# Optimization experiments

Measured on AMD Instinct MI355X. Metric: run time of the kernel, lower is better.

Reference implementation:

```python
import jax, jax.numpy as jnp
import numpy as np

N = 524288            # total ray samples
EMB_DIM = 32          # hash embedder out_dim (16 levels x 2 feats)
DIR_DIM = 27          # freq embedder out_dim (3 + 3*2*4)
GEO_FEAT = 15         # cfg.geo_feature_dim
LATENT_DIM = 128      # cfg.latent_code_dim
NUM_LATENT = 100      # cfg.num_latent_code
D_HIDDEN = 64
RGB_IN = EMB_DIM + DIR_DIM + GEO_FEAT + LATENT_DIM  # 202


def setup_inputs() -> dict:
    key = jax.random.key(0)
    ks = jax.random.split(key, 16)

    def lin(k, fan_in, fan_out):
        # torch nn.Linear default init: U(-1/sqrt(fan_in), 1/sqrt(fan_in))
        bound = 1.0 / np.sqrt(fan_in)
        kw, kb = jax.random.split(k)
        W = jax.random.uniform(kw, (fan_in, fan_out), jnp.float32, -bound, bound)
        b = jax.random.uniform(kb, (fan_out,), jnp.float32, -bound, bound)
        return W, b

    occ_W0, occ_b0 = lin(ks[0], EMB_DIM, D_HIDDEN)
    occ_W1, occ_b1 = lin(ks[1], D_HIDDEN, D_HIDDEN)
    occ_W2, occ_b2 = lin(ks[2], D_HIDDEN, 1 + GEO_FEAT)
    rgb_W0, rgb_b0 = lin(ks[3], RGB_IN, D_HIDDEN)
    rgb_W1, rgb_b1 = lin(ks[4], D_HIDDEN, D_HIDDEN)
    rgb_W2, rgb_b2 = lin(ks[5], D_HIDDEN, 3)

    # kaiming_normal_ init of rgb_latent
    rgb_latent = jax.random.normal(ks[6], (NUM_LATENT, LATENT_DIM), jnp.float32) * np.sqrt(2.0 / LATENT_DIM)

    embedded = jax.random.normal(ks[7], (N, EMB_DIM), jnp.float32)
    embedded_dir = jax.random.normal(ks[8], (N, DIR_DIM), jnp.float32)

    return {
        'embedded': embedded, 'embedded_dir': embedded_dir,
        'occ_W0': occ_W0, 'occ_b0': occ_b0,
        'occ_W1': occ_W1, 'occ_b1': occ_b1,
        'occ_W2': occ_W2, 'occ_b2': occ_b2,
        'rgb_W0': rgb_W0, 'rgb_b0': rgb_b0,
        'rgb_W1': rgb_W1, 'rgb_b1': rgb_b1,
        'rgb_W2': rgb_W2, 'rgb_b2': rgb_b2,
        'rgb_latent': rgb_latent,
        'latent_index': 7,
    }


def reference(embedded, embedded_dir,
              occ_W0, occ_b0, occ_W1, occ_b1, occ_W2, occ_b2,
              rgb_W0, rgb_b0, rgb_W1, rgb_b1, rgb_W2, rgb_b2,
              rgb_latent, latent_index):
    sp = jax.nn.softplus
    # occ MLP: softplus hidden layers, linear output
    h = sp(embedded @ occ_W0 + occ_b0)
    h = sp(h @ occ_W1 + occ_b1)
    hidden = h @ occ_W2 + occ_b2                     # [N, 1+GEO_FEAT]
    occ = 1.0 - jnp.exp(-sp(hidden[:, :1]))          # [N, 1]
    feature = hidden[:, 1:]                          # [N, GEO_FEAT]
    # latent gather: one latent code broadcast over all N samples
    n = embedded.shape[0]
    latent = jnp.broadcast_to(rgb_latent[latent_index], (n, rgb_latent.shape[1]))
    x = jnp.concatenate([embedded, embedded_dir, feature, latent], axis=-1)  # [N, 202]
    # rgb MLP
    r = sp(x @ rgb_W0 + rgb_b0)
    r = sp(r @ rgb_W1 + rgb_b1)
    rgb = jax.nn.sigmoid(r @ rgb_W2 + rgb_b2)        # [N, 3]
    raw = jnp.concatenate([rgb, occ], axis=-1)       # [N, 4]
    return raw, occ
```

## Files before the change

### kernel.cpp

```cpp
#include <hip/hip_runtime.h>

typedef __bf16 bf16x8 __attribute__((ext_vector_type(8)));
typedef float f32x4 __attribute__((ext_vector_type(4)));
typedef unsigned int u32x4 __attribute__((ext_vector_type(4)));
typedef unsigned int u32x2 __attribute__((ext_vector_type(2)));
typedef u32x4 u32x4a __attribute__((may_alias));
typedef u32x2 u32x2a __attribute__((may_alias));
typedef f32x4 f32x4a __attribute__((may_alias));

#define NITER 8

__device__ inline unsigned short f2b(float f) {
    unsigned int x;
    __builtin_memcpy(&x, &f, 4);
    unsigned int r = (x + 0x7FFFu + ((x >> 16) & 1u)) >> 16;
    return (unsigned short)r;
}
__device__ inline unsigned int cvt_pk_bf16(float lo, float hi) {
    unsigned int r;
    asm("v_cvt_pk_bf16_f32 %0, %1, %2" : "=v"(r) : "v"(lo), "v"(hi));
    return r;
}
__device__ inline float softplus_f(float x) {
    return fmaxf(x, 0.f) + __logf(1.f + __expf(-fabsf(x)));
}
__device__ inline bf16x8 as_bf16x8(u32x4 v) { return __builtin_bit_cast(bf16x8, v); }


__global__ __launch_bounds__(256) void prep_weights(
    const float* __restrict__ oW0, const float* __restrict__ ob0,
    const float* __restrict__ oW1, const float* __restrict__ ob1,
    const float* __restrict__ oW2, const float* __restrict__ ob2,
    const float* __restrict__ rW0, const float* __restrict__ rb0,
    const float* __restrict__ rW1, const float* __restrict__ rb1,
    const float* __restrict__ rW2, const float* __restrict__ rb2,
    const float* __restrict__ rlat, const int* __restrict__ lidx,
    float* __restrict__ wsf, ushort* __restrict__ wsw)
{
    const int tid = threadIdx.x;
    for (int i = tid; i < 224; i += 256) {
        float v;
        if (i < 64)       v = ob0[i];
        else if (i < 128) v = ob1[i - 64];
        else if (i < 144) v = ob2[i - 128];
        else if (i < 208) v = rb1[i - 144];
        else              v = (i - 208 < 3) ? rb2[i - 208] : 0.f;
        wsf[i] = v;
    }
    if (tid < 64) {
        float acc = rb0[tid];
        const float* lat = rlat + (size_t)lidx[0] * 128;
        for (int k = 0; k < 128; k++)
            acc = fmaf(lat[k], rW0[(74 + k) * 64 + tid], acc);
        wsf[224 + tid] = acc;
    }
    for (int s = tid; s < 36 * 64; s += 256) {
        const int frag = s >> 6, lane = s & 63;
        const int qq = lane >> 4, cc = lane & 15;
        const float* W;
        int ldn = 64, nt = 0, kt = 0;
        bool isr0 = false, isr2 = false;
        if (frag < 4)       { W = oW0; nt = frag; kt = 0; }
        else if (frag < 12) { W = oW1; int f = frag - 4;  nt = f >> 1; kt = f & 1; }
        else if (frag < 14) { W = oW2; ldn = 16; nt = 0; kt = frag - 12; }
        else if (frag < 26) { W = rW0; int f = frag - 14; nt = f / 3; kt = f - nt * 3; isr0 = true; }
        else if (frag < 34) { W = rW1; int f = frag - 26; nt = f >> 1; kt = f & 1; }
        else                { W = rW2; ldn = 3; nt = 0; kt = frag - 34; isr2 = true; }
        const int nn = nt * 16 + cc;
        __align__(16) ushort vals[8];
#pragma unroll
        for (int j = 0; j < 8; j++) {
            int k = kt * 32 + qq * 8 + j;
            float v = 0.f;
            if (isr0) {
                int ks = -1;
                if (k < 59) ks = k;
                else if (k >= 64 && k < 79) ks = k - 5;
                if (ks >= 0) v = W[ks * 64 + nn];
            } else if (isr2) {
                if (nn < 3) v = W[k * 3 + nn];
            } else {
                v = W[k * ldn + nn];
            }
            vals[j] = f2b(v);
        }
        *(u32x4a*)&wsw[s * 8] = *(const u32x4a*)vals;
    }
}

__global__ __launch_bounds__(512, 4) void net_mfma(
    const float* __restrict__ emb, const float* __restrict__ dir,
    const float* __restrict__ wsf, const ushort* __restrict__ wsw,
    float* __restrict__ out, int n)
{
    __shared__ __align__(16) ushort s_w[36 * 64 * 8];
    __shared__ __align__(16) float  s_bias[288];
    __shared__ __align__(16) ushort s_h[8][16 * 72];
    __shared__ __align__(16) ushort s_feat[8][16 * 24];

    const int tid = threadIdx.x;
    for (int i = tid; i < 36 * 64; i += 512)
        *(u32x4a*)&s_w[i * 8] = *(const u32x4a*)(wsw + i * 8);
    for (int i = tid; i < 288; i += 512)
        s_bias[i] = wsf[i];
    __syncthreads();

    const int wave = tid >> 6, lane = tid & 63, q = lane >> 4, c = lane & 15;
    ushort* hw = s_h[wave];
    ushort* fw = s_feat[wave];
    if (lane < 16) fw[lane * 24 + 15] = 0;

    for (int it = 0; it < NITER; ++it) {
        const long p0 = (long)blockIdx.x * 1024 + it * 128 + wave * 16;

        bf16x8 x_emb, x_dir;
        {
            const float* ep = emb + (p0 + c) * 32 + q * 8;
            f32x4 e0 = *(const f32x4a*)ep;
            f32x4 e1 = *(const f32x4a*)(ep + 4);
            u32x4 pk = {cvt_pk_bf16(e0[0], e0[1]), cvt_pk_bf16(e0[2], e0[3]),
                        cvt_pk_bf16(e1[0], e1[1]), cvt_pk_bf16(e1[2], e1[3])};
            x_emb = as_bf16x8(pk);
        }
        {
            const float* dp = dir + (p0 + c) * 27;
            float dv[8];
#pragma unroll
            for (int j = 0; j < 8; j++) {
                int kl = q * 8 + j;
                dv[j] = (kl < 27) ? dp[kl] : 0.f;
            }
            u32x4 pk = {cvt_pk_bf16(dv[0], dv[1]), cvt_pk_bf16(dv[2], dv[3]),
                        cvt_pk_bf16(dv[4], dv[5]), cvt_pk_bf16(dv[6], dv[7])};
            x_dir = as_bf16x8(pk);
        }

#pragma unroll
        for (int nt = 0; nt < 4; ++nt) {
            f32x4 acc = *(const f32x4a*)&s_bias[0 + nt * 16 + q * 4];
            acc = __builtin_amdgcn_mfma_f32_16x16x32_bf16(
                as_bf16x8(*(const u32x4a*)&s_w[((0 + nt) * 64 + lane) * 8]), x_emb, acc, 0, 0, 0);
            u32x2 pk = {cvt_pk_bf16(softplus_f(acc[0]), softplus_f(acc[1])),
                        cvt_pk_bf16(softplus_f(acc[2]), softplus_f(acc[3]))};
            *(u32x2a*)&hw[c * 72 + nt * 16 + q * 4] = pk;
        }
        {
            bf16x8 h0 = as_bf16x8(*(const u32x4a*)&hw[c * 72 + 0 + q * 8]);
            bf16x8 h1 = as_bf16x8(*(const u32x4a*)&hw[c * 72 + 32 + q * 8]);
#pragma unroll
            for (int nt = 0; nt < 4; ++nt) {
                f32x4 acc = *(const f32x4a*)&s_bias[64 + nt * 16 + q * 4];
                acc = __builtin_amdgcn_mfma_f32_16x16x32_bf16(
                    as_bf16x8(*(const u32x4a*)&s_w[((4 + nt * 2 + 0) * 64 + lane) * 8]), h0, acc, 0, 0, 0);
                acc = __builtin_amdgcn_mfma_f32_16x16x32_bf16(
                    as_bf16x8(*(const u32x4a*)&s_w[((4 + nt * 2 + 1) * 64 + lane) * 8]), h1, acc, 0, 0, 0);
                u32x2 pk = {cvt_pk_bf16(softplus_f(acc[0]), softplus_f(acc[1])),
                            cvt_pk_bf16(softplus_f(acc[2]), softplus_f(acc[3]))};
                *(u32x2a*)&hw[c * 72 + nt * 16 + q * 4] = pk;
            }
        }
        float occv;
        {
            bf16x8 h0 = as_bf16x8(*(const u32x4a*)&hw[c * 72 + 0 + q * 8]);
            bf16x8 h1 = as_bf16x8(*(const u32x4a*)&hw[c * 72 + 32 + q * 8]);
            f32x4 acc = *(const f32x4a*)&s_bias[128 + q * 4];
            acc = __builtin_amdgcn_mfma_f32_16x16x32_bf16(
                as_bf16x8(*(const u32x4a*)&s_w[(12 * 64 + lane) * 8]), h0, acc, 0, 0, 0);
            acc = __builtin_amdgcn_mfma_f32_16x16x32_bf16(
                as_bf16x8(*(const u32x4a*)&s_w[(13 * 64 + lane) * 8]), h1, acc, 0, 0, 0);
            occv = 1.f - __expf(-softplus_f(acc[0]));
#pragma unroll
            for (int r = 0; r < 4; r++) {
                int o = q * 4 + r;
                if (o > 0) fw[c * 24 + o - 1] = f2b(acc[r]);
            }
        }
        {
            u32x4 rawf = *(const u32x4a*)&fw[c * 24 + q * 8];
            if (q >= 2) rawf = u32x4{0, 0, 0, 0};
            bf16x8 x_feat = as_bf16x8(rawf);
#pragma unroll
            for (int nt = 0; nt < 4; ++nt) {
                f32x4 acc = *(const f32x4a*)&s_bias[224 + nt * 16 + q * 4];
                acc = __builtin_amdgcn_mfma_f32_16x16x32_bf16(
                    as_bf16x8(*(const u32x4a*)&s_w[((14 + nt * 3 + 0) * 64 + lane) * 8]), x_emb, acc, 0, 0, 0);
                acc = __builtin_amdgcn_mfma_f32_16x16x32_bf16(
                    as_bf16x8(*(const u32x4a*)&s_w[((14 + nt * 3 + 1) * 64 + lane) * 8]), x_dir, acc, 0, 0, 0);
                acc = __builtin_amdgcn_mfma_f32_16x16x32_bf16(
                    as_bf16x8(*(const u32x4a*)&s_w[((14 + nt * 3 + 2) * 64 + lane) * 8]), x_feat, acc, 0, 0, 0);
                u32x2 pk = {cvt_pk_bf16(softplus_f(acc[0]), softplus_f(acc[1])),
                            cvt_pk_bf16(softplus_f(acc[2]), softplus_f(acc[3]))};
                *(u32x2a*)&hw[c * 72 + nt * 16 + q * 4] = pk;
            }
        }
        {
            bf16x8 h0 = as_bf16x8(*(const u32x4a*)&hw[c * 72 + 0 + q * 8]);
            bf16x8 h1 = as_bf16x8(*(const u32x4a*)&hw[c * 72 + 32 + q * 8]);
#pragma unroll
            for (int nt = 0; nt < 4; ++nt) {
                f32x4 acc = *(const f32x4a*)&s_bias[144 + nt * 16 + q * 4];
                acc = __builtin_amdgcn_mfma_f32_16x16x32_bf16(
                    as_bf16x8(*(const u32x4a*)&s_w[((26 + nt * 2 + 0) * 64 + lane) * 8]), h0, acc, 0, 0, 0);
                acc = __builtin_amdgcn_mfma_f32_16x16x32_bf16(
                    as_bf16x8(*(const u32x4a*)&s_w[((26 + nt * 2 + 1) * 64 + lane) * 8]), h1, acc, 0, 0, 0);
                u32x2 pk = {cvt_pk_bf16(softplus_f(acc[0]), softplus_f(acc[1])),
                            cvt_pk_bf16(softplus_f(acc[2]), softplus_f(acc[3]))};
                *(u32x2a*)&hw[c * 72 + nt * 16 + q * 4] = pk;
            }
        }
        {
            bf16x8 h0 = as_bf16x8(*(const u32x4a*)&hw[c * 72 + 0 + q * 8]);
            bf16x8 h1 = as_bf16x8(*(const u32x4a*)&hw[c * 72 + 32 + q * 8]);
            f32x4 acc = *(const f32x4a*)&s_bias[208 + q * 4];
            acc = __builtin_amdgcn_mfma_f32_16x16x32_bf16(
                as_bf16x8(*(const u32x4a*)&s_w[(34 * 64 + lane) * 8]), h0, acc, 0, 0, 0);
            acc = __builtin_amdgcn_mfma_f32_16x16x32_bf16(
                as_bf16x8(*(const u32x4a*)&s_w[(35 * 64 + lane) * 8]), h1, acc, 0, 0, 0);
            if (q == 0) {
                f32x4 o;
                o[0] = 1.f / (1.f + __expf(-acc[0]));
                o[1] = 1.f / (1.f + __expf(-acc[1]));
                o[2] = 1.f / (1.f + __expf(-acc[2]));
                o[3] = occv;
                *(f32x4a*)&out[(p0 + c) * 4] = o;
                out[(long)4 * n + p0 + c] = occv;
            }
        }
    }
}

extern "C" void kernel_launch(void* const* d_in, const int* in_sizes, int n_in,
                              void* d_out, int out_size, void* d_ws, size_t ws_size,
                              hipStream_t stream) {
    const int n = in_sizes[0] / 32;
    float*  wsf = (float*)d_ws;
    ushort* wsw = (ushort*)((char*)d_ws + 1152);
    prep_weights<<<1, 256, 0, stream>>>(
        (const float*)d_in[2], (const float*)d_in[3],
        (const float*)d_in[4], (const float*)d_in[5],
        (const float*)d_in[6], (const float*)d_in[7],
        (const float*)d_in[8], (const float*)d_in[9],
        (const float*)d_in[10], (const float*)d_in[11],
        (const float*)d_in[12], (const float*)d_in[13],
        (const float*)d_in[14], (const int*)d_in[15],
        wsf, wsw);
    net_mfma<<<n / 1024, 512, 0, stream>>>(
        (const float*)d_in[0], (const float*)d_in[1],
        wsf, wsw, (float*)d_out, n);
}
```

Baseline: 235.5 us.

## Streamline activations, keep biases in registers, vectorize dir loads, parallelize weight prep

Replaces softplus and sigmoid with raw v_exp/v_log/v_rcp intrinsics and computes occupancy as sigmoid(x), using the identity 1-exp(-softplus(x)) = sigmoid(x). Biases move from LDS into registers. The feature vector is repacked in place in the hidden buffer by shifting the rgb_W0 layout, which removes the separate feature LDS buffer. The direction loads become vectorized float4 loads with a bounds fallback, and weight prep is spread over 8 blocks with a split reduction for the latent dot product. The unguarded softplus form log2(1+exp2(x)) can overflow for large inputs, and the extra bias registers raise register pressure.

```diff
diff --git a/kernel.cpp b/kernel.cpp
--- a/kernel.cpp
+++ b/kernel.cpp
@@ -7,6 +7,7 @@
 typedef u32x4 u32x4a __attribute__((may_alias));
 typedef u32x2 u32x2a __attribute__((may_alias));
 typedef f32x4 f32x4a __attribute__((may_alias));
+typedef unsigned int u32a __attribute__((may_alias));
 
 #define NITER 8
 
@@ -21,8 +22,14 @@
     asm("v_cvt_pk_bf16_f32 %0, %1, %2" : "=v"(r) : "v"(lo), "v"(hi));
     return r;
 }
+__device__ inline float vexp2(float x) { float r; asm("v_exp_f32 %0, %1" : "=v"(r) : "v"(x)); return r; }
+__device__ inline float vlog2(float x) { float r; asm("v_log_f32 %0, %1" : "=v"(r) : "v"(x)); return r; }
+__device__ inline float vrcp(float x)  { float r; asm("v_rcp_f32 %0, %1" : "=v"(r) : "v"(x)); return r; }
 __device__ inline float softplus_f(float x) {
-    return fmaxf(x, 0.f) + __logf(1.f + __expf(-fabsf(x)));
+    return 0.69314718f * vlog2(1.f + vexp2(1.44269504f * x));
+}
+__device__ inline float sigmoid_f(float x) {
+    return vrcp(1.f + vexp2(-1.44269504f * x));
 }
 __device__ inline bf16x8 as_bf16x8(u32x4 v) { return __builtin_bit_cast(bf16x8, v); }
 
@@ -37,24 +44,33 @@
     const float* __restrict__ rlat, const int* __restrict__ lidx,
     float* __restrict__ wsf, ushort* __restrict__ wsw)
 {
-    const int tid = threadIdx.x;
-    for (int i = tid; i < 224; i += 256) {
-        float v;
-        if (i < 64)       v = ob0[i];
-        else if (i < 128) v = ob1[i - 64];
-        else if (i < 144) v = ob2[i - 128];
-        else if (i < 208) v = rb1[i - 144];
-        else              v = (i - 208 < 3) ? rb2[i - 208] : 0.f;
-        wsf[i] = v;
-    }
-    if (tid < 64) {
-        float acc = rb0[tid];
+    const int bid = blockIdx.x, tid = threadIdx.x;
+    __shared__ float red[256];
+
+    if (bid == 0) {
+        for (int i = tid; i < 224; i += 256) {
+            float v;
+            if (i < 64)       v = ob0[i];
+            else if (i < 128) v = ob1[i - 64];
+            else if (i < 144) v = ob2[i - 128];
+            else if (i < 208) v = rb1[i - 144];
+            else              v = (i - 208 < 3) ? rb2[i - 208] : 0.f;
+            wsf[i] = v;
+        }
+    }
+    if (bid == 7) {
+        const int outn = tid & 63, sl = tid >> 6;
         const float* lat = rlat + (size_t)lidx[0] * 128;
-        for (int k = 0; k < 128; k++)
-            acc = fmaf(lat[k], rW0[(74 + k) * 64 + tid], acc);
-        wsf[224 + tid] = acc;
-    }
-    for (int s = tid; s < 36 * 64; s += 256) {
+        float p = 0.f;
+        for (int k = sl * 32; k < sl * 32 + 32; k++)
+            p = fmaf(lat[k], rW0[(74 + k) * 64 + outn], p);
+        red[tid] = p;
+        __syncthreads();
+        if (tid < 64)
+            wsf[224 + tid] = rb0[tid] + red[tid] + red[64 + tid] + red[128 + tid] + red[192 + tid];
+    }
+    for (int t = tid; t < 288; t += 256) {
+        const int s = bid * 288 + t;
         const int frag = s >> 6, lane = s & 63;
         const int qq = lane >> 4, cc = lane & 15;
         const float* W;
@@ -75,7 +91,7 @@
             if (isr0) {
                 int ks = -1;
                 if (k < 59) ks = k;
-                else if (k >= 64 && k < 79) ks = k - 5;
+                else if (k >= 65 && k < 80) ks = k - 65 + 59;
                 if (ks >= 0) v = W[ks * 64 + nn];
             } else if (isr2) {
                 if (nn < 3) v = W[k * 3 + nn];
@@ -94,21 +110,30 @@
     float* __restrict__ out, int n)
 {
     __shared__ __align__(16) ushort s_w[36 * 64 * 8];
-    __shared__ __align__(16) float  s_bias[288];
     __shared__ __align__(16) ushort s_h[8][16 * 72];
-    __shared__ __align__(16) ushort s_feat[8][16 * 24];
 
     const int tid = threadIdx.x;
     for (int i = tid; i < 36 * 64; i += 512)
         *(u32x4a*)&s_w[i * 8] = *(const u32x4a*)(wsw + i * 8);
-    for (int i = tid; i < 288; i += 512)
-        s_bias[i] = wsf[i];
     __syncthreads();
 
     const int wave = tid >> 6, lane = tid & 63, q = lane >> 4, c = lane & 15;
     ushort* hw = s_h[wave];
-    ushort* fw = s_feat[wave];
-    if (lane < 16) fw[lane * 24 + 15] = 0;
+    for (int i = lane; i < 576; i += 64) ((u32a*)hw)[i] = 0u;
+
+    const int q4 = q * 4;
+    f32x4 Bv[18];
+#pragma unroll
+    for (int nt = 0; nt < 4; nt++) {
+        Bv[0 + nt]  = *(const f32x4a*)(wsf + 0   + nt * 16 + q4);
+        Bv[4 + nt]  = *(const f32x4a*)(wsf + 64  + nt * 16 + q4);
+        Bv[9 + nt]  = *(const f32x4a*)(wsf + 224 + nt * 16 + q4);
+        Bv[13 + nt] = *(const f32x4a*)(wsf + 144 + nt * 16 + q4);
+    }
+    Bv[8]  = *(const f32x4a*)(wsf + 128 + q4);
+    Bv[17] = *(const f32x4a*)(wsf + 208 + q4);
+
+    const long dlim = (long)n * 27;
 
     for (int it = 0; it < NITER; ++it) {
         const long p0 = (long)blockIdx.x * 1024 + it * 128 + wave * 16;
@@ -123,65 +148,64 @@
             x_emb = as_bf16x8(pk);
         }
         {
-            const float* dp = dir + (p0 + c) * 27;
-            float dv[8];
-#pragma unroll
-            for (int j = 0; j < 8; j++) {
-                int kl = q * 8 + j;
-                dv[j] = (kl < 27) ? dp[kl] : 0.f;
-            }
-            u32x4 pk = {cvt_pk_bf16(dv[0], dv[1]), cvt_pk_bf16(dv[2], dv[3]),
-                        cvt_pk_bf16(dv[4], dv[5]), cvt_pk_bf16(dv[6], dv[7])};
+            const long ib = (p0 + c) * 27 + q * 8;
+            f32x4 d0, d1;
+            if (ib + 8 <= dlim) {
+                d0 = *(const f32x4a*)(dir + ib);
+                d1 = *(const f32x4a*)(dir + ib + 4);
+            } else {
+#pragma unroll
+                for (int j = 0; j < 4; j++) d0[j] = (ib + j < dlim) ? dir[ib + j] : 0.f;
+#pragma unroll
+                for (int j = 0; j < 4; j++) d1[j] = (ib + 4 + j < dlim) ? dir[ib + 4 + j] : 0.f;
+            }
+            u32x4 pk = {cvt_pk_bf16(d0[0], d0[1]), cvt_pk_bf16(d0[2], d0[3]),
+                        cvt_pk_bf16(d1[0], d1[1]), cvt_pk_bf16(d1[2], d1[3])};
             x_dir = as_bf16x8(pk);
         }
 
 #pragma unroll
         for (int nt = 0; nt < 4; ++nt) {
-            f32x4 acc = *(const f32x4a*)&s_bias[0 + nt * 16 + q * 4];
+            f32x4 acc = Bv[0 + nt];
             acc = __builtin_amdgcn_mfma_f32_16x16x32_bf16(
                 as_bf16x8(*(const u32x4a*)&s_w[((0 + nt) * 64 + lane) * 8]), x_emb, acc, 0, 0, 0);
             u32x2 pk = {cvt_pk_bf16(softplus_f(acc[0]), softplus_f(acc[1])),
                         cvt_pk_bf16(softplus_f(acc[2]), softplus_f(acc[3]))};
-            *(u32x2a*)&hw[c * 72 + nt * 16 + q * 4] = pk;
+            *(u32x2a*)&hw[c * 72 + nt * 16 + q4] = pk;
         }
         {
             bf16x8 h0 = as_bf16x8(*(const u32x4a*)&hw[c * 72 + 0 + q * 8]);
             bf16x8 h1 = as_bf16x8(*(const u32x4a*)&hw[c * 72 + 32 + q * 8]);
 #pragma unroll
             for (int nt = 0; nt < 4; ++nt) {
-                f32x4 acc = *(const f32x4a*)&s_bias[64 + nt * 16 + q * 4];
+                f32x4 acc = Bv[4 + nt];
                 acc = __builtin_amdgcn_mfma_f32_16x16x32_bf16(
                     as_bf16x8(*(const u32x4a*)&s_w[((4 + nt * 2 + 0) * 64 + lane) * 8]), h0, acc, 0, 0, 0);
                 acc = __builtin_amdgcn_mfma_f32_16x16x32_bf16(
                     as_bf16x8(*(const u32x4a*)&s_w[((4 + nt * 2 + 1) * 64 + lane) * 8]), h1, acc, 0, 0, 0);
                 u32x2 pk = {cvt_pk_bf16(softplus_f(acc[0]), softplus_f(acc[1])),
                             cvt_pk_bf16(softplus_f(acc[2]), softplus_f(acc[3]))};
-                *(u32x2a*)&hw[c * 72 + nt * 16 + q * 4] = pk;
+                *(u32x2a*)&hw[c * 72 + nt * 16 + q4] = pk;
             }
         }
         float occv;
         {
             bf16x8 h0 = as_bf16x8(*(const u32x4a*)&hw[c * 72 + 0 + q * 8]);
             bf16x8 h1 = as_bf16x8(*(const u32x4a*)&hw[c * 72 + 32 + q * 8]);
-            f32x4 acc = *(const f32x4a*)&s_bias[128 + q * 4];
+            f32x4 acc = Bv[8];
             acc = __builtin_amdgcn_mfma_f32_16x16x32_bf16(
                 as_bf16x8(*(const u32x4a*)&s_w[(12 * 64 + lane) * 8]), h0, acc, 0, 0, 0);
             acc = __builtin_amdgcn_mfma_f32_16x16x32_bf16(
                 as_bf16x8(*(const u32x4a*)&s_w[(13 * 64 + lane) * 8]), h1, acc, 0, 0, 0);
-            occv = 1.f - __expf(-softplus_f(acc[0]));
-#pragma unroll
-            for (int r = 0; r < 4; r++) {
-                int o = q * 4 + r;
-                if (o > 0) fw[c * 24 + o - 1] = f2b(acc[r]);
-            }
-        }
-        {
-            u32x4 rawf = *(const u32x4a*)&fw[c * 24 + q * 8];
-            if (q >= 2) rawf = u32x4{0, 0, 0, 0};
-            bf16x8 x_feat = as_bf16x8(rawf);
+            occv = sigmoid_f(acc[0]);
+            u32x2 pk = {cvt_pk_bf16(acc[0], acc[1]), cvt_pk_bf16(acc[2], acc[3])};
+            *(u32x2a*)&hw[c * 72 + q4] = pk;
+        }
+        {
+            bf16x8 x_feat = as_bf16x8(*(const u32x4a*)&hw[c * 72 + q * 8]);
 #pragma unroll
             for (int nt = 0; nt < 4; ++nt) {
-                f32x4 acc = *(const f32x4a*)&s_bias[224 + nt * 16 + q * 4];
+                f32x4 acc = Bv[9 + nt];
                 acc = __builtin_amdgcn_mfma_f32_16x16x32_bf16(
                     as_bf16x8(*(const u32x4a*)&s_w[((14 + nt * 3 + 0) * 64 + lane) * 8]), x_emb, acc, 0, 0, 0);
                 acc = __builtin_amdgcn_mfma_f32_16x16x32_bf16(
@@ -190,7 +214,7 @@
                     as_bf16x8(*(const u32x4a*)&s_w[((14 + nt * 3 + 2) * 64 + lane) * 8]), x_feat, acc, 0, 0, 0);
                 u32x2 pk = {cvt_pk_bf16(softplus_f(acc[0]), softplus_f(acc[1])),
                             cvt_pk_bf16(softplus_f(acc[2]), softplus_f(acc[3]))};
-                *(u32x2a*)&hw[c * 72 + nt * 16 + q * 4] = pk;
+                *(u32x2a*)&hw[c * 72 + nt * 16 + q4] = pk;
             }
         }
         {
@@ -198,29 +222,29 @@
             bf16x8 h1 = as_bf16x8(*(const u32x4a*)&hw[c * 72 + 32 + q * 8]);
 #pragma unroll
             for (int nt = 0; nt < 4; ++nt) {
-                f32x4 acc = *(const f32x4a*)&s_bias[144 + nt * 16 + q * 4];
+                f32x4 acc = Bv[13 + nt];
                 acc = __builtin_amdgcn_mfma_f32_16x16x32_bf16(
                     as_bf16x8(*(const u32x4a*)&s_w[((26 + nt * 2 + 0) * 64 + lane) * 8]), h0, acc, 0, 0, 0);
                 acc = __builtin_amdgcn_mfma_f32_16x16x32_bf16(
                     as_bf16x8(*(const u32x4a*)&s_w[((26 + nt * 2 + 1) * 64 + lane) * 8]), h1, acc, 0, 0, 0);
                 u32x2 pk = {cvt_pk_bf16(softplus_f(acc[0]), softplus_f(acc[1])),
                             cvt_pk_bf16(softplus_f(acc[2]), softplus_f(acc[3]))};
-                *(u32x2a*)&hw[c * 72 + nt * 16 + q * 4] = pk;
-            }
-        }
-        {
-            bf16x8 h0 = as_bf16x8(*(const u32x4a*)&hw[c * 72 + 0 + q * 8]);
-            bf16x8 h1 = as_bf16x8(*(const u32x4a*)&hw[c * 72 + 32 + q * 8]);
-            f32x4 acc = *(const f32x4a*)&s_bias[208 + q * 4];
+                *(u32x2a*)&hw[c * 72 + nt * 16 + q4] = pk;
+            }
+        }
+        {
+            bf16x8 h0 = as_bf16x8(*(const u32x4a*)&hw[c * 72 + 0 + q * 8]);
+            bf16x8 h1 = as_bf16x8(*(const u32x4a*)&hw[c * 72 + 32 + q * 8]);
+            f32x4 acc = Bv[17];
             acc = __builtin_amdgcn_mfma_f32_16x16x32_bf16(
                 as_bf16x8(*(const u32x4a*)&s_w[(34 * 64 + lane) * 8]), h0, acc, 0, 0, 0);
             acc = __builtin_amdgcn_mfma_f32_16x16x32_bf16(
                 as_bf16x8(*(const u32x4a*)&s_w[(35 * 64 + lane) * 8]), h1, acc, 0, 0, 0);
             if (q == 0) {
                 f32x4 o;
-                o[0] = 1.f / (1.f + __expf(-acc[0]));
-                o[1] = 1.f / (1.f + __expf(-acc[1]));
-                o[2] = 1.f / (1.f + __expf(-acc[2]));
+                o[0] = sigmoid_f(acc[0]);
+                o[1] = sigmoid_f(acc[1]);
+                o[2] = sigmoid_f(acc[2]);
                 o[3] = occv;
                 *(f32x4a*)&out[(p0 + c) * 4] = o;
                 out[(long)4 * n + p0 + c] = occv;
@@ -235,7 +259,7 @@
     const int n = in_sizes[0] / 32;
     float*  wsf = (float*)d_ws;
     ushort* wsw = (ushort*)((char*)d_ws + 1152);
-    prep_weights<<<1, 256, 0, stream>>>(
+    prep_weights<<<8, 256, 0, stream>>>(
         (const float*)d_in[2], (const float*)d_in[3],
         (const float*)d_in[4], (const float*)d_in[5],
         (const float*)d_in[6], (const float*)d_in[7],
```

Measured after the change: 195.3 us. -17.0%, faster.
